# Performance work log

Hardware: AMD Instinct MI355X
Metric: run time of the kernel (lower is better)

Reference implementation:

```python
import jax, jax.numpy as jnp
import numpy as np

B, N, F, C, E = 32768, 14, 128, 128, 64
NEG_SLOPE = 0.2

def setup_inputs() -> dict:
    key = jax.random.key(0)
    ks = jax.random.split(key, 14)
    feature = jax.random.normal(ks[0], (B, N, F), jnp.float32)
    src = jax.random.randint(ks[1], (B, E), 0, N)
    off = jax.random.randint(ks[2], (B, E), 1, N)
    dst = (src + off) % N  # guaranteed no self loops
    edge_list = jnp.stack([src, dst], axis=-1)  # [B,E,2] (src,dst) pairs
    s = 0.1
    return {
        'feature': feature,
        'edge_list': edge_list,
        'W1': jax.random.normal(ks[3], (F, C), jnp.float32) * s,
        'a_s1': jax.random.normal(ks[4], (C,), jnp.float32) * s,
        'a_d1': jax.random.normal(ks[5], (C,), jnp.float32) * s,
        'b1': jnp.zeros((C,), jnp.float32),
        'W2': jax.random.normal(ks[6], (C, C), jnp.float32) * s,
        'a_s2': jax.random.normal(ks[7], (C,), jnp.float32) * s,
        'a_d2': jax.random.normal(ks[8], (C,), jnp.float32) * s,
        'b2': jnp.zeros((C,), jnp.float32),
        'Wl': jax.random.normal(ks[9], (N * C, C // 2), jnp.float32) * 0.02,
        'bl': jnp.zeros((C // 2,), jnp.float32),
        'Wp': jax.random.normal(ks[10], (C // 2, 1), jnp.float32) * 0.02,
        'bp': jnp.zeros((1,), jnp.float32),
    }

def _gat_layer(x, W, a_s, a_d, b, src, dst):
    # x: [B,N,Fin]; src,dst: [B,Et] (self loops included). PyG GATConv, 1 head.
    Bn, Nn, _ = x.shape
    Et = src.shape[1]
    h = x @ W                                   # [B,N,C]
    as_n = jnp.einsum('bnc,c->bn', h, a_s)      # per-node src score
    ad_n = jnp.einsum('bnc,c->bn', h, a_d)      # per-node dst score
    logit = jax.nn.leaky_relu(
        jnp.take_along_axis(as_n, src, axis=1) + jnp.take_along_axis(ad_n, dst, axis=1),
        NEG_SLOPE)                               # [B,Et]
    # edge softmax grouped by (graph, dst) via flat segment ids
    seg = (jnp.arange(Bn)[:, None] * Nn + dst).reshape(-1)   # [B*Et]
    lf = logit.reshape(-1)
    m = jnp.full((Bn * Nn,), -jnp.inf, lf.dtype).at[seg].max(lf)
    e = jnp.exp(lf - m[seg])
    z = jnp.zeros((Bn * Nn,), lf.dtype).at[seg].add(e)
    alpha = e / z[seg]                           # [B*Et]
    Cc = h.shape[-1]
    msg = jnp.take_along_axis(h, src[..., None], axis=1).reshape(Bn * Et, Cc) * alpha[:, None]
    out = jnp.zeros((Bn * Nn, Cc), h.dtype).at[seg].add(msg).reshape(Bn, Nn, Cc) + b
    return out, alpha.reshape(Bn, Et)

def reference(feature, edge_list, W1, a_s1, a_d1, b1, W2, a_s2, a_d2, b2, Wl, bl, Wp, bp):
    Bn = feature.shape[0]
    sl = jnp.broadcast_to(jnp.arange(N)[None, :], (Bn, N))
    src = jnp.concatenate([edge_list[..., 0], sl], axis=1)   # [B,E+N]
    dst = jnp.concatenate([edge_list[..., 1], sl], axis=1)
    h1, _ = _gat_layer(feature, W1, a_s1, a_d1, b1, src, dst)
    h1 = jax.nn.relu(h1)                         # dropout p=0 (eval)
    h2, alpha = _gat_layer(h1, W2, a_s2, a_d2, b2, src, dst)
    attn = jnp.zeros((Bn, N, N), feature.dtype).at[jnp.arange(Bn)[:, None], src, dst].set(alpha)
    x = h2.reshape(Bn, N * C) @ Wl + bl
    pred = jax.nn.sigmoid(x @ Wp + bp)           # [B,1]
    return pred, attn
```

## Files before the change

### kernel.cpp

```cpp
#include <hip/hip_runtime.h>


#define NEG_SLOPE 0.2f

typedef __bf16 bf16x8 __attribute__((ext_vector_type(8)));
typedef float f32x4 __attribute__((ext_vector_type(4)));
typedef unsigned short us4v __attribute__((ext_vector_type(4)));
typedef unsigned short us8v __attribute__((ext_vector_type(8)));

static __device__ __forceinline__ unsigned short f2bf(float f) {
  unsigned u = __builtin_bit_cast(unsigned, f);
  return (unsigned short)((u + 0x7FFFu + ((u >> 16) & 1u)) >> 16);
}

__global__ void gat_setup_kernel(const float* __restrict__ W1, const float* __restrict__ W2,
                                 const float* __restrict__ Wl, const float* __restrict__ bl,
                                 const float* __restrict__ Wp, const float* __restrict__ bp,
                                 unsigned short* __restrict__ wfrag, float* __restrict__ weffc) {
  const int blk = blockIdx.x, tid = threadIdx.x;
  if (blk < 16) {
    int slot = blk * 256 + tid;
    int lane = slot & 63, t = (slot >> 6) & 7, ks = (slot >> 9) & 3, lr = slot >> 11;
    const float* W = lr ? W2 : W1;
    int q = lane >> 4, l = lane & 15;
    int n = t * 16 + l, k0 = ks * 32 + q * 8;
    us8v hv;
    #pragma unroll
    for (int j = 0; j < 8; ++j) hv[j] = f2bf(W[(k0 + j) * 128 + n]);
    *(us8v*)(wfrag + slot * 8) = hv;
  } else {
    for (int i = tid; i < 2048; i += 256) {
      int r = i & 3, lane = (i >> 2) & 63, t = i >> 8;
      int q = lane >> 4, l = lane & 15;
      int row = 4 * q + r, col = t * 16 + l;
      float s = 0.f;
      if (row < 14) {
        const float* wl = Wl + (size_t)(row * 128 + col) * 64;
        #pragma unroll 8
        for (int c = 0; c < 64; ++c) s += wl[c] * Wp[c];
      }
      weffc[i] = s;
    }
    if (tid == 0) {
      float s = 0.f;
      for (int c = 0; c < 64; ++c) s += bl[c] * Wp[c];
      weffc[2048] = s + bp[0];
    }
  }
}

struct __align__(16) WaveLds {
  unsigned short xh[2176];
  unsigned short Pb[256];
  float Pf[224];
  float asn[16], adn[16], mz[16];
  int emask[16];
};

__global__ __launch_bounds__(1024, 4) void gat_kernel(
    const float* __restrict__ feat, const int* __restrict__ edges,
    const float* __restrict__ as1v, const float* __restrict__ ad1v,
    const float* __restrict__ b1v, const float* __restrict__ as2v,
    const float* __restrict__ ad2v, const float* __restrict__ b2v,
    const unsigned short* __restrict__ wfrag, const float* __restrict__ weffc,
    float* __restrict__ out) {
  __shared__ unsigned short sW[32768];
  __shared__ WaveLds wls[16];

  const int tid = threadIdx.x;
  const int wave = tid >> 6, lane = tid & 63;
  const int q = lane >> 4, l = lane & 15;
  const int g = blockIdx.x * 16 + wave;
  WaveLds& S = wls[wave];

  f32x4 fv[8];
  if (l < 14) {
    const float* fb = feat + (size_t)g * 1792 + l * 128 + q * 8;
    #pragma unroll
    for (int ks = 0; ks < 4; ++ks) {
      fv[2 * ks] = *(const f32x4*)(fb + ks * 32);
      fv[2 * ks + 1] = *(const f32x4*)(fb + ks * 32 + 4);
    }
  } else {
    #pragma unroll
    for (int c = 0; c < 8; ++c) fv[c] = (f32x4){0.f, 0.f, 0.f, 0.f};
  }
  int esrc, edst;
  { const int2 e2 = *(const int2*)(edges + (size_t)g * 128 + lane * 2); esrc = e2.x; edst = e2.y; }
  if (lane < 16) S.emask[lane] = 0;

  #pragma unroll
  for (int it = 0; it < 4; ++it) {
    int off = it * 1024 + tid;
    *(us8v*)(&sW[off * 8]) = *(const us8v*)(wfrag + off * 8);
  }
  __syncthreads();

  atomicOr(&S.emask[esrc], 1 << edst);
  if (lane < 14) atomicOr(&S.emask[lane], 1 << lane);

  us8v z8v = {0, 0, 0, 0, 0, 0, 0, 0};
  const bf16x8 zf = __builtin_bit_cast(bf16x8, z8v);

  bf16x8 af1[4];
  #pragma unroll
  for (int ks = 0; ks < 4; ++ks) {
    us8v hv;
    hv[0] = f2bf(fv[2 * ks][0]); hv[1] = f2bf(fv[2 * ks][1]);
    hv[2] = f2bf(fv[2 * ks][2]); hv[3] = f2bf(fv[2 * ks][3]);
    hv[4] = f2bf(fv[2 * ks + 1][0]); hv[5] = f2bf(fv[2 * ks + 1][1]);
    hv[6] = f2bf(fv[2 * ks + 1][2]); hv[7] = f2bf(fv[2 * ks + 1][3]);
    af1[ks] = __builtin_bit_cast(bf16x8, hv);
  }

  f32x4 oacc[8];

  for (int lr = 0; lr < 2; ++lr) {
    const float* asv = lr ? as2v : as1v;
    const float* adv = lr ? ad2v : ad1v;
    const float* bsv = lr ? b2v : b1v;

    f32x4 hacc[8];
    #pragma unroll
    for (int t = 0; t < 8; ++t) hacc[t] = (f32x4){0.f, 0.f, 0.f, 0.f};
    #pragma unroll
    for (int ks = 0; ks < 4; ++ks) {
      bf16x8 af = lr ? *(const bf16x8*)(&S.xh[l * 136 + ks * 32 + q * 8]) : af1[ks];
      const unsigned short* wk = sW + (lr * 4 + ks) * 4096 + lane * 8;
      #pragma unroll
      for (int t = 0; t < 8; ++t) {
        bf16x8 bfv = *(const bf16x8*)(wk + t * 512);
        hacc[t] = __builtin_amdgcn_mfma_f32_16x16x32_bf16(af, bfv, hacc[t], 0, 0, 0);
      }
    }

    f32x4 pas = {0.f, 0.f, 0.f, 0.f}, padv = {0.f, 0.f, 0.f, 0.f};
    #pragma unroll
    for (int t = 0; t < 8; ++t) {
      float ca = asv[t * 16 + l], cd = adv[t * 16 + l];
      pas += hacc[t] * ca;
      padv += hacc[t] * cd;
    }
    #pragma unroll
    for (int m = 1; m <= 8; m <<= 1) {
      #pragma unroll
      for (int r = 0; r < 4; ++r) {
        pas[r] += __shfl_xor(pas[r], m, 64);
        padv[r] += __shfl_xor(padv[r], m, 64);
      }
    }
    if (l == 0) {
      #pragma unroll
      for (int r = 0; r < 4; ++r) { S.asn[4 * q + r] = pas[r]; S.adn[4 * q + r] = padv[r]; }
    }

    #pragma unroll
    for (int t = 0; t < 8; ++t) {
      us4v hv;
      hv[0] = f2bf(hacc[t][0]); hv[1] = f2bf(hacc[t][1]);
      hv[2] = f2bf(hacc[t][2]); hv[3] = f2bf(hacc[t][3]);
      *(us4v*)(&S.xh[(t * 16 + l) * 16 + q * 4]) = hv;
    }
    if (lane < 56) *(f32x4*)(&S.Pf[lane * 4]) = (f32x4){0.f, 0.f, 0.f, 0.f};
    __threadfence_block();

    float f0 = S.asn[esrc] + S.adn[edst];
    float ev = __expf(f0 > 0.f ? f0 : NEG_SLOPE * f0);
    atomicAdd(&S.Pf[edst * 16 + esrc], ev);
    if (lane < 14) {
      float f2 = S.asn[lane] + S.adn[lane];
      atomicAdd(&S.Pf[lane * 17], __expf(f2 > 0.f ? f2 : NEG_SLOPE * f2));
    }
    __threadfence_block();

    if (lane < 14) {
      f32x4 s0 = *(const f32x4*)(&S.Pf[lane * 16]) + *(const f32x4*)(&S.Pf[lane * 16 + 4]) +
                 *(const f32x4*)(&S.Pf[lane * 16 + 8]) + *(const f32x4*)(&S.Pf[lane * 16 + 12]);
      S.mz[lane] = 1.f / (s0[0] + s0[1] + s0[2] + s0[3]);
    }
    __threadfence_block();

    #pragma unroll
    for (int i = lane; i < 256; i += 64) {
      int r = i >> 4, c = i & 15;
      S.Pb[i] = (r < 14 && c < 14) ? f2bf(S.Pf[i] * S.mz[r]) : (unsigned short)0;
    }
    __threadfence_block();

    #pragma unroll
    for (int t = 0; t < 8; ++t) {
      float bb = bsv[t * 16 + l];
      oacc[t] = (f32x4){bb, bb, bb, bb};
    }
    bf16x8 paf = (q < 2) ? *(const bf16x8*)(&S.Pb[l * 16 + q * 8]) : zf;
    #pragma unroll
    for (int t = 0; t < 8; ++t) {
      bf16x8 hbf = (q < 2) ? *(const bf16x8*)(&S.xh[(t * 16 + l) * 16 + q * 8]) : zf;
      oacc[t] = __builtin_amdgcn_mfma_f32_16x16x32_bf16(paf, hbf, oacc[t], 0, 0, 0);
    }

    if (lr == 0) {
      __threadfence_block();
      #pragma unroll
      for (int t = 0; t < 8; ++t) {
        #pragma unroll
        for (int r = 0; r < 4; ++r) {
          float v = fmaxf(oacc[t][r], 0.f);
          S.xh[(4 * q + r) * 136 + t * 16 + l] = f2bf(v);
        }
      }
      __threadfence_block();
    }
  }

  float part = 0.f;
  #pragma unroll
  for (int t = 0; t < 8; ++t) {
    f32x4 wv = *(const f32x4*)(weffc + t * 256 + lane * 4);
    part += oacc[t][0] * wv[0] + oacc[t][1] * wv[1] + oacc[t][2] * wv[2] + oacc[t][3] * wv[3];
  }
  #pragma unroll
  for (int m = 1; m < 64; m <<= 1) part += __shfl_xor(part, m, 64);
  if (lane == 0) out[g] = 1.f / (1.f + __expf(-(part + weffc[2048])));

  {
    float* oa = out + 32768 + (size_t)g * 196;
    #pragma unroll
    for (int k = 0; k < 4; ++k) {
      int i = lane + k * 64;
      if (i < 196) {
        int s = (i * 4682) >> 16;
        int d = i - s * 14;
        float a = 0.f;
        if ((S.emask[s] >> d) & 1) {
          float f = S.asn[s] + S.adn[d];
          a = __expf(f > 0.f ? f : NEG_SLOPE * f) * S.mz[d];
        }
        oa[i] = a;
      }
    }
  }
}

extern "C" void kernel_launch(void* const* d_in, const int* in_sizes, int n_in,
                              void* d_out, int out_size, void* d_ws, size_t ws_size,
                              hipStream_t stream) {
  const float* feat = (const float*)d_in[0];
  const int* edges = (const int*)d_in[1];
  const float* W1 = (const float*)d_in[2];
  const float* as1 = (const float*)d_in[3];
  const float* ad1 = (const float*)d_in[4];
  const float* b1 = (const float*)d_in[5];
  const float* W2 = (const float*)d_in[6];
  const float* as2 = (const float*)d_in[7];
  const float* ad2 = (const float*)d_in[8];
  const float* b2 = (const float*)d_in[9];
  const float* Wl = (const float*)d_in[10];
  const float* bl = (const float*)d_in[11];
  const float* Wp = (const float*)d_in[12];
  const float* bp = (const float*)d_in[13];

  unsigned short* wfrag = (unsigned short*)d_ws;
  float* weffc = (float*)((char*)d_ws + 65536);

  gat_setup_kernel<<<17, 256, 0, stream>>>(W1, W2, Wl, bl, Wp, bp, wfrag, weffc);
  gat_kernel<<<2048, 1024, 0, stream>>>(feat, edges, as1, ad1, b1, as2, ad2, b2,
                                        wfrag, weffc, (float*)d_out);
}
```

Measured before the change: 490.7 us.

## Fold attention vectors into weight MFMA and read weights from global

Precomputes W·a_s and W·a_d in the setup kernel as an extra ninth MFMA column tile, so per-node attention scores come out of the projection MFMA and the shuffle reduction goes away. Drops the 64KB shared-memory weight staging and its block barrier, reading weight fragments directly from global/L2, and shrinks blocks to 512 threads with more blocks per CU. Also removes the intermediate bf16 probability buffer by normalizing and converting in registers before the aggregation MFMA. The trade is more global/L2 weight traffic per wave, plus scores now computed in bf16, which lowers precision.

```diff
diff --git a/kernel.cpp b/kernel.cpp
--- a/kernel.cpp
+++ b/kernel.cpp
@@ -14,19 +14,36 @@
 }
 
 __global__ void gat_setup_kernel(const float* __restrict__ W1, const float* __restrict__ W2,
+                                 const float* __restrict__ as1, const float* __restrict__ ad1,
+                                 const float* __restrict__ as2, const float* __restrict__ ad2,
                                  const float* __restrict__ Wl, const float* __restrict__ bl,
                                  const float* __restrict__ Wp, const float* __restrict__ bp,
                                  unsigned short* __restrict__ wfrag, float* __restrict__ weffc) {
   const int blk = blockIdx.x, tid = threadIdx.x;
-  if (blk < 16) {
+  if (blk < 18) {
     int slot = blk * 256 + tid;
-    int lane = slot & 63, t = (slot >> 6) & 7, ks = (slot >> 9) & 3, lr = slot >> 11;
+    int lane = slot & 63, frag = slot >> 6;
+    int lr = frag / 36, rem = frag % 36, ks = rem / 9, t = rem % 9;
     const float* W = lr ? W2 : W1;
     int q = lane >> 4, l = lane & 15;
-    int n = t * 16 + l, k0 = ks * 32 + q * 8;
+    int k0 = ks * 32 + q * 8;
     us8v hv;
-    #pragma unroll
-    for (int j = 0; j < 8; ++j) hv[j] = f2bf(W[(k0 + j) * 128 + n]);
+    if (t < 8) {
+      int n = t * 16 + l;
+      #pragma unroll
+      for (int j = 0; j < 8; ++j) hv[j] = f2bf(W[(k0 + j) * 128 + n]);
+    } else {
+      const float* vec = l ? (lr ? ad2 : ad1) : (lr ? as2 : as1);
+      #pragma unroll
+      for (int j = 0; j < 8; ++j) {
+        float s = 0.f;
+        if (l < 2) {
+          const float* wr = W + (size_t)(k0 + j) * 128;
+          for (int c = 0; c < 128; ++c) s += wr[c] * vec[c];
+        }
+        hv[j] = f2bf(s);
+      }
+    }
     *(us8v*)(wfrag + slot * 8) = hv;
   } else {
     for (int i = tid; i < 2048; i += 256) {
@@ -51,107 +68,70 @@
 
 struct __align__(16) WaveLds {
   unsigned short xh[2176];
-  unsigned short Pb[256];
-  float Pf[224];
+  float Pf[256];
   float asn[16], adn[16], mz[16];
   int emask[16];
 };
 
-__global__ __launch_bounds__(1024, 4) void gat_kernel(
+__global__ __launch_bounds__(512, 6) void gat_kernel(
     const float* __restrict__ feat, const int* __restrict__ edges,
-    const float* __restrict__ as1v, const float* __restrict__ ad1v,
-    const float* __restrict__ b1v, const float* __restrict__ as2v,
-    const float* __restrict__ ad2v, const float* __restrict__ b2v,
+    const float* __restrict__ b1v, const float* __restrict__ b2v,
     const unsigned short* __restrict__ wfrag, const float* __restrict__ weffc,
     float* __restrict__ out) {
-  __shared__ unsigned short sW[32768];
-  __shared__ WaveLds wls[16];
-
+  __shared__ WaveLds wls[8];
   const int tid = threadIdx.x;
   const int wave = tid >> 6, lane = tid & 63;
   const int q = lane >> 4, l = lane & 15;
-  const int g = blockIdx.x * 16 + wave;
+  const int g = blockIdx.x * 8 + wave;
   WaveLds& S = wls[wave];
 
-  f32x4 fv[8];
+  us8v z8v = {0, 0, 0, 0, 0, 0, 0, 0};
+  const bf16x8 zf = __builtin_bit_cast(bf16x8, z8v);
+
+  bf16x8 af1[4];
   if (l < 14) {
     const float* fb = feat + (size_t)g * 1792 + l * 128 + q * 8;
     #pragma unroll
     for (int ks = 0; ks < 4; ++ks) {
-      fv[2 * ks] = *(const f32x4*)(fb + ks * 32);
-      fv[2 * ks + 1] = *(const f32x4*)(fb + ks * 32 + 4);
+      f32x4 v0 = *(const f32x4*)(fb + ks * 32);
+      f32x4 v1 = *(const f32x4*)(fb + ks * 32 + 4);
+      us8v hv;
+      hv[0] = f2bf(v0[0]); hv[1] = f2bf(v0[1]); hv[2] = f2bf(v0[2]); hv[3] = f2bf(v0[3]);
+      hv[4] = f2bf(v1[0]); hv[5] = f2bf(v1[1]); hv[6] = f2bf(v1[2]); hv[7] = f2bf(v1[3]);
+      af1[ks] = __builtin_bit_cast(bf16x8, hv);
     }
   } else {
     #pragma unroll
-    for (int c = 0; c < 8; ++c) fv[c] = (f32x4){0.f, 0.f, 0.f, 0.f};
+    for (int ks = 0; ks < 4; ++ks) af1[ks] = zf;
   }
   int esrc, edst;
   { const int2 e2 = *(const int2*)(edges + (size_t)g * 128 + lane * 2); esrc = e2.x; edst = e2.y; }
   if (lane < 16) S.emask[lane] = 0;
 
-  #pragma unroll
-  for (int it = 0; it < 4; ++it) {
-    int off = it * 1024 + tid;
-    *(us8v*)(&sW[off * 8]) = *(const us8v*)(wfrag + off * 8);
-  }
-  __syncthreads();
-
-  atomicOr(&S.emask[esrc], 1 << edst);
-  if (lane < 14) atomicOr(&S.emask[lane], 1 << lane);
-
-  us8v z8v = {0, 0, 0, 0, 0, 0, 0, 0};
-  const bf16x8 zf = __builtin_bit_cast(bf16x8, z8v);
-
-  bf16x8 af1[4];
-  #pragma unroll
-  for (int ks = 0; ks < 4; ++ks) {
-    us8v hv;
-    hv[0] = f2bf(fv[2 * ks][0]); hv[1] = f2bf(fv[2 * ks][1]);
-    hv[2] = f2bf(fv[2 * ks][2]); hv[3] = f2bf(fv[2 * ks][3]);
-    hv[4] = f2bf(fv[2 * ks + 1][0]); hv[5] = f2bf(fv[2 * ks + 1][1]);
-    hv[6] = f2bf(fv[2 * ks + 1][2]); hv[7] = f2bf(fv[2 * ks + 1][3]);
-    af1[ks] = __builtin_bit_cast(bf16x8, hv);
-  }
-
   f32x4 oacc[8];
 
   for (int lr = 0; lr < 2; ++lr) {
-    const float* asv = lr ? as2v : as1v;
-    const float* adv = lr ? ad2v : ad1v;
     const float* bsv = lr ? b2v : b1v;
 
-    f32x4 hacc[8];
-    #pragma unroll
-    for (int t = 0; t < 8; ++t) hacc[t] = (f32x4){0.f, 0.f, 0.f, 0.f};
+    f32x4 hacc[9];
+    #pragma unroll
+    for (int t = 0; t < 9; ++t) hacc[t] = (f32x4){0.f, 0.f, 0.f, 0.f};
     #pragma unroll
     for (int ks = 0; ks < 4; ++ks) {
       bf16x8 af = lr ? *(const bf16x8*)(&S.xh[l * 136 + ks * 32 + q * 8]) : af1[ks];
-      const unsigned short* wk = sW + (lr * 4 + ks) * 4096 + lane * 8;
+      const unsigned short* wk = wfrag + ((lr * 4 + ks) * 9) * 512 + lane * 8;
       #pragma unroll
       for (int t = 0; t < 8; ++t) {
         bf16x8 bfv = *(const bf16x8*)(wk + t * 512);
         hacc[t] = __builtin_amdgcn_mfma_f32_16x16x32_bf16(af, bfv, hacc[t], 0, 0, 0);
       }
-    }
-
-    f32x4 pas = {0.f, 0.f, 0.f, 0.f}, padv = {0.f, 0.f, 0.f, 0.f};
-    #pragma unroll
-    for (int t = 0; t < 8; ++t) {
-      float ca = asv[t * 16 + l], cd = adv[t * 16 + l];
-      pas += hacc[t] * ca;
-      padv += hacc[t] * cd;
-    }
-    #pragma unroll
-    for (int m = 1; m <= 8; m <<= 1) {
-      #pragma unroll
-      for (int r = 0; r < 4; ++r) {
-        pas[r] += __shfl_xor(pas[r], m, 64);
-        padv[r] += __shfl_xor(padv[r], m, 64);
-      }
-    }
-    if (l == 0) {
-      #pragma unroll
-      for (int r = 0; r < 4; ++r) { S.asn[4 * q + r] = pas[r]; S.adn[4 * q + r] = padv[r]; }
+      bf16x8 bsc = (l < 2) ? *(const bf16x8*)(wk + 8 * 512) : zf;
+      hacc[8] = __builtin_amdgcn_mfma_f32_16x16x32_bf16(af, bsc, hacc[8], 0, 0, 0);
+    }
+
+    if (l < 2) {
+      float* dst = l ? S.adn : S.asn;
+      *(f32x4*)(dst + 4 * q) = hacc[8];
     }
 
     #pragma unroll
@@ -161,29 +141,25 @@
       hv[2] = f2bf(hacc[t][2]); hv[3] = f2bf(hacc[t][3]);
       *(us4v*)(&S.xh[(t * 16 + l) * 16 + q * 4]) = hv;
     }
-    if (lane < 56) *(f32x4*)(&S.Pf[lane * 4]) = (f32x4){0.f, 0.f, 0.f, 0.f};
+    *(f32x4*)(&S.Pf[lane * 4]) = (f32x4){0.f, 0.f, 0.f, 0.f};
     __threadfence_block();
 
     float f0 = S.asn[esrc] + S.adn[edst];
     float ev = __expf(f0 > 0.f ? f0 : NEG_SLOPE * f0);
     atomicAdd(&S.Pf[edst * 16 + esrc], ev);
+    if (lr == 0) atomicOr(&S.emask[esrc], 1 << edst);
     if (lane < 14) {
       float f2 = S.asn[lane] + S.adn[lane];
       atomicAdd(&S.Pf[lane * 17], __expf(f2 > 0.f ? f2 : NEG_SLOPE * f2));
+      if (lr == 0) atomicOr(&S.emask[lane], 1 << lane);
     }
     __threadfence_block();
 
-    if (lane < 14) {
+    if (lane < 16) {
       f32x4 s0 = *(const f32x4*)(&S.Pf[lane * 16]) + *(const f32x4*)(&S.Pf[lane * 16 + 4]) +
                  *(const f32x4*)(&S.Pf[lane * 16 + 8]) + *(const f32x4*)(&S.Pf[lane * 16 + 12]);
-      S.mz[lane] = 1.f / (s0[0] + s0[1] + s0[2] + s0[3]);
-    }
-    __threadfence_block();
-
-    #pragma unroll
-    for (int i = lane; i < 256; i += 64) {
-      int r = i >> 4, c = i & 15;
-      S.Pb[i] = (r < 14 && c < 14) ? f2bf(S.Pf[i] * S.mz[r]) : (unsigned short)0;
+      float z = s0[0] + s0[1] + s0[2] + s0[3];
+      S.mz[lane] = (lane < 14) ? 1.f / z : 0.f;
     }
     __threadfence_block();
 
@@ -192,7 +168,18 @@
       float bb = bsv[t * 16 + l];
       oacc[t] = (f32x4){bb, bb, bb, bb};
     }
-    bf16x8 paf = (q < 2) ? *(const bf16x8*)(&S.Pb[l * 16 + q * 8]) : zf;
+    bf16x8 paf = zf;
+    if (q < 2) {
+      f32x4 p0 = *(const f32x4*)(&S.Pf[l * 16 + q * 8]);
+      f32x4 p1 = *(const f32x4*)(&S.Pf[l * 16 + q * 8 + 4]);
+      float m = S.mz[l];
+      us8v pv;
+      pv[0] = f2bf(p0[0] * m); pv[1] = f2bf(p0[1] * m);
+      pv[2] = f2bf(p0[2] * m); pv[3] = f2bf(p0[3] * m);
+      pv[4] = f2bf(p1[0] * m); pv[5] = f2bf(p1[1] * m);
+      pv[6] = f2bf(p1[2] * m); pv[7] = f2bf(p1[3] * m);
+      paf = __builtin_bit_cast(bf16x8, pv);
+    }
     #pragma unroll
     for (int t = 0; t < 8; ++t) {
       bf16x8 hbf = (q < 2) ? *(const bf16x8*)(&S.xh[(t * 16 + l) * 16 + q * 8]) : zf;
@@ -261,9 +248,10 @@
   const float* bp = (const float*)d_in[13];
 
   unsigned short* wfrag = (unsigned short*)d_ws;
-  float* weffc = (float*)((char*)d_ws + 65536);
-
-  gat_setup_kernel<<<17, 256, 0, stream>>>(W1, W2, Wl, bl, Wp, bp, wfrag, weffc);
-  gat_kernel<<<2048, 1024, 0, stream>>>(feat, edges, as1, ad1, b1, as2, ad2, b2,
-                                        wfrag, weffc, (float*)d_out);
-}
+  float* weffc = (float*)((char*)d_ws + 73728);
+
+  gat_setup_kernel<<<19, 256, 0, stream>>>(W1, W2, as1, ad1, as2, ad2,
+                                           Wl, bl, Wp, bp, wfrag, weffc);
+  gat_kernel<<<4096, 512, 0, stream>>>(feat, edges, b1, b2, wfrag, weffc,
+                                       (float*)d_out);
+}
```

After: 576.4 us. 17.5% more time.
